# Optimization experiments

Hardware: AMD Instinct MI355X
Metric: run time of the kernel (lower is better)

The kernel has to match this reference:

```python
import jax, jax.numpy as jnp
import numpy as np

HEADS = 8
DIM_HEAD = 64
SCALE = DIM_HEAD ** -0.5


def setup_inputs() -> dict:
    key = jax.random.key(0)
    k1, k2, k3 = jax.random.split(key, 3)
    b, n, dim = 2, 4096, 512
    inner = HEADS * DIM_HEAD
    x = jax.random.normal(k1, (b, n, dim), dtype=jnp.float32)
    w_qkv = jax.random.normal(k2, (dim, 3 * inner), dtype=jnp.float32) * (dim ** -0.5)
    w_out = jax.random.normal(k3, (inner, dim), dtype=jnp.float32) * (inner ** -0.5)
    b_out = jnp.zeros((dim,), dtype=jnp.float32)
    return {"x": x, "w_qkv": w_qkv, "w_out": w_out, "b_out": b_out}


def reference(x, w_qkv, w_out, b_out):
    b, n, dim = x.shape
    qkv = x @ w_qkv  # [b, n, 3*inner]
    q, k, v = jnp.split(qkv, 3, axis=-1)
    # b n (h d) -> b h n d
    split_heads = lambda t: t.reshape(b, n, HEADS, DIM_HEAD).transpose(0, 2, 1, 3)
    q, k, v = split_heads(q), split_heads(k), split_heads(v)
    dots = jnp.einsum('bhid,bhjd->bhij', q, k) * SCALE  # [b, h, n, n]
    attn = jax.nn.log_softmax(dots, axis=-1)  # NOTE: log-softmax, not softmax
    out = jnp.einsum('bhij,bhjd->bhid', attn, v)  # [b, h, n, d]
    out = out.transpose(0, 2, 1, 3).reshape(b, n, HEADS * DIM_HEAD)
    return out @ w_out + b_out + x
```

## Files before the change

kernel.cpp:

```cpp
#include <hip/hip_runtime.h>
#include <stdint.h>

#define NSEQ   4096
#define BATCH  2
#define NHEAD  8
#define DHEAD  64
#define DIM    512
#define NQKV   1536
#define MROWS  (BATCH*NSEQ)
#define NBH    (BATCH*NHEAD)

typedef float  f32x4 __attribute__((ext_vector_type(4)));
typedef short  s16x8 __attribute__((ext_vector_type(8)));

__device__ __forceinline__ unsigned short f2b(float f){
  unsigned int u = __float_as_uint(f);
  u += 0x7FFFu + ((u >> 16) & 1u);
  return (unsigned short)(u >> 16);
}
__device__ __forceinline__ float b2f(unsigned short h){
  return __uint_as_float(((unsigned int)h) << 16);
}
__device__ __forceinline__ void gld_lds16(const void* g, void* l){
  __builtin_amdgcn_global_load_lds((const __attribute__((address_space(1))) unsigned int*)g,
                                   (__attribute__((address_space(3))) unsigned int*)l, 16, 0, 0);
}

__global__ void k_prep(const float* __restrict__ x, unsigned short* __restrict__ xb,
                       const float* __restrict__ wqkv, unsigned short* __restrict__ wqT,
                       const float* __restrict__ wout, unsigned short* __restrict__ woT){
  __shared__ float t[32][33];
  const int b = blockIdx.x;
  if (b < 4096){
    const int i = b*256 + threadIdx.x;
    float4 v = ((const float4*)x)[i];
    ushort4 o;
    o.x = f2b(v.x); o.y = f2b(v.y); o.z = f2b(v.z); o.w = f2b(v.w);
    ((ushort4*)xb)[i] = o;
  } else {
    const float* in; unsigned short* out; int R, C, cb, rb;
    if (b < 4096 + 768){
      const int q = b - 4096; in = wqkv; out = wqT; R = DIM; C = NQKV;
      cb = (q % 48)*32; rb = (q / 48)*32;
    } else {
      const int q = b - 4096 - 768; in = wout; out = woT; R = DIM; C = DIM;
      cb = (q & 15)*32; rb = (q >> 4)*32;
    }
    const int tx = threadIdx.x & 31, ty = threadIdx.x >> 5;
    #pragma unroll
    for (int s = 0; s < 32; s += 8) t[ty+s][tx] = in[(size_t)(rb+ty+s)*C + cb + tx];
    __syncthreads();
    #pragma unroll
    for (int s = 0; s < 32; s += 8) out[(size_t)(cb+ty+s)*R + rb + tx] = f2b(t[tx][ty+s]);
  }
}

#define QSTAGE(KS, B) do{ \
    const int k0_ = (KS)*32; \
    _Pragma("unroll") \
    for (int i_ = 0; i_ < 2; ++i_){ \
      const int slot_ = w*2 + i_; \
      const int r_ = slot_*16 + (lane>>2); \
      const int ch_ = (lane&3) ^ (r_&3); \
      gld_lds16(A  + (size_t)(m0+r_)*DIM + k0_ + ch_*8, (char*)at[B] + slot_*1024); \
      gld_lds16(Bt + (size_t)(n0+r_)*DIM + k0_ + ch_*8, (char*)bt[B] + slot_*1024); \
    }}while(0)

__global__ __launch_bounds__(256) void k_qkv_gemm(
    const unsigned short* __restrict__ A,
    const unsigned short* __restrict__ Bt,
    unsigned short* __restrict__ qbuf, unsigned short* __restrict__ kbuf,
    unsigned short* __restrict__ vbuf){
  __shared__ __align__(16) unsigned short at[2][128*32];
  __shared__ __align__(16) unsigned short bt[2][128*32];
  const int n0 = blockIdx.x*128, m0 = blockIdx.y*128;
  const int tid = threadIdx.x, w = tid>>6, lane = tid&63;
  const int wr = (w>>1)*64, wc = (w&1)*64;
  f32x4 acc[4][4] = {};
  QSTAGE(0, 0);
  for (int ks = 0; ks < 16; ++ks){
    __syncthreads();
    if (ks < 15) QSTAGE(ks+1, (ks+1)&1);
    const unsigned short* atc = at[ks&1];
    const unsigned short* btc = bt[ks&1];
    s16x8 af[4], bfr[4];
    #pragma unroll
    for (int f = 0; f < 4; ++f){
      const int rr = wr + f*16 + (lane&15);
      af[f]  = *(const s16x8*)((const char*)atc + rr*64 + ((((lane>>4)) ^ (rr&3))<<4));
      const int cc = wc + f*16 + (lane&15);
      bfr[f] = *(const s16x8*)((const char*)btc + cc*64 + ((((lane>>4)) ^ (cc&3))<<4));
    }
    #pragma unroll
    for (int fr = 0; fr < 4; ++fr)
      #pragma unroll
      for (int fc = 0; fc < 4; ++fc)
        acc[fr][fc] = __builtin_amdgcn_mfma_f32_16x16x32_bf16(bfr[fc], af[fr], acc[fr][fc], 0,0,0);
  }
  const float QS = 0.18033688011112042f;
  #pragma unroll
  for (int fr = 0; fr < 4; ++fr){
    const int row = m0 + wr + fr*16 + (lane&15);
    const int b = row >> 12, n = row & 4095;
    #pragma unroll
    for (int fc = 0; fc < 4; ++fc){
      const int col0 = n0 + wc + fc*16 + ((lane>>4)<<2);
      const int which = col0 >> 9;
      const int h = (col0 & 511) >> 6;
      const int d = col0 & 63;
      unsigned short* dst = (which==0) ? qbuf : ((which==1) ? kbuf : vbuf);
      const float sc = (which==0) ? QS : 1.f;
      ushort4 o;
      o.x = f2b(acc[fr][fc][0]*sc);
      o.y = f2b(acc[fr][fc][1]*sc);
      o.z = f2b(acc[fr][fc][2]*sc);
      o.w = f2b(acc[fr][fc][3]*sc);
      *(ushort4*)(dst + (size_t)((b*NHEAD + h)*NSEQ + n)*DHEAD + d) = o;
    }
  }
}

__global__ __launch_bounds__(256) void k_tpart(
    const unsigned short* __restrict__ kbuf, const unsigned short* __restrict__ vbuf,
    unsigned short* __restrict__ tpart, float* __restrict__ vsp){
  __shared__ __align__(16) unsigned short kt[64*64];
  __shared__ __align__(16) unsigned short vt[64*64];
  const int bh = blockIdx.y, jc = blockIdx.x;
  const unsigned short* K = kbuf + (size_t)bh*NSEQ*DHEAD;
  const unsigned short* V = vbuf + (size_t)bh*NSEQ*DHEAD;
  const int tid = threadIdx.x;
  const int d1 = (tid>>4)<<2, d2 = (tid&15)<<2;
  const int j0 = jc*64;
  #pragma unroll
  for (int c = 0; c < 2; ++c){
    const int q = tid + 256*c;
    const int row = q>>3, ch = q&7;
    *(float4*)((char*)kt + row*128 + ch*16) = *(const float4*)((const char*)K + (size_t)(j0+row)*128 + ch*16);
    *(float4*)((char*)vt + row*128 + ch*16) = *(const float4*)((const char*)V + (size_t)(j0+row)*128 + ch*16);
  }
  __syncthreads();
  float accT[4][4] = {{0.f}};
  float accV[4] = {0.f,0.f,0.f,0.f};
  for (int jj = 0; jj < 64; ++jj){
    const ushort4 k4 = *(const ushort4*)(kt + jj*64 + d1);
    const ushort4 v4 = *(const ushort4*)(vt + jj*64 + d2);
    float kf[4] = {b2f(k4.x), b2f(k4.y), b2f(k4.z), b2f(k4.w)};
    float vf[4] = {b2f(v4.x), b2f(v4.y), b2f(v4.z), b2f(v4.w)};
    #pragma unroll
    for (int a = 0; a < 4; ++a)
      #pragma unroll
      for (int b = 0; b < 4; ++b) accT[a][b] += kf[a]*vf[b];
    #pragma unroll
    for (int b = 0; b < 4; ++b) accV[b] += vf[b];
  }
  unsigned short* tp = tpart + ((size_t)bh*64 + jc)*4096;
  #pragma unroll
  for (int a = 0; a < 4; ++a)
    #pragma unroll
    for (int b = 0; b < 4; ++b) tp[(d1+a)*64 + (d2+b)] = f2b(accT[a][b]);
  if (tid < 16){
    #pragma unroll
    for (int b = 0; b < 4; ++b) vsp[((size_t)bh*64 + jc)*64 + d2 + b] = accV[b];
  }
}

__global__ void k_tred(const unsigned short* __restrict__ tpart, const float* __restrict__ vsp,
                       unsigned short* __restrict__ TB, float* __restrict__ vsum){
  const int blk = blockIdx.x;
  const int bh = blk >> 4, part = blk & 15;
  const int tid = threadIdx.x;
  const int idx = part*256 + tid;
  const int dd1 = idx>>6, dd2 = idx&63;
  float s = 0.f;
  #pragma unroll 8
  for (int pr = 0; pr < 64; ++pr) s += b2f(tpart[((size_t)bh*64 + pr)*4096 + idx]);
  TB[(size_t)bh*4096 + dd2*64 + dd1] = f2b(s);
  if (part == 0 && tid < 64){
    float v = 0.f;
    #pragma unroll 8
    for (int pr = 0; pr < 64; ++pr) v += vsp[((size_t)bh*64 + pr)*64 + tid];
    vsum[bh*64 + tid] = v;
  }
}

#define ASTAGE(U, BUFI) do { \
    const int ti_ = jbase + (((U)+phase)&15); \
    const size_t o_ = (size_t)ti_*64*DHEAD; \
    char* d_ = (char*)kt[BUFI]; \
    gld_lds16(kg0 + o_, d_ + s0*1024); \
    gld_lds16(kg1 + o_, d_ + s1*1024); } while(0)

#define ATILE(BUF) do { \
    const char* buf_ = (const char*)(BUF); \
    _Pragma("unroll") \
    for (int kk = 0; kk < 4; ++kk){ \
      const int r_ = kk*16 + (lane&15); \
      const s16x8 b0_ = *(const s16x8*)(buf_ + r_*128 + ((((lane>>4))   ^ (r_&7))<<4)); \
      const s16x8 b1_ = *(const s16x8*)(buf_ + r_*128 + (((4+(lane>>4)) ^ (r_&7))<<4)); \
      f32x4 a0_ = {0.f,0.f,0.f,0.f}, a1_ = {0.f,0.f,0.f,0.f}; \
      f32x4 a2_ = {0.f,0.f,0.f,0.f}, a3_ = {0.f,0.f,0.f,0.f}; \
      __builtin_amdgcn_s_setprio(1); \
      a0_ = __builtin_amdgcn_mfma_f32_16x16x32_bf16(aq[0][0], b0_, a0_, 0,0,0); \
      a0_ = __builtin_amdgcn_mfma_f32_16x16x32_bf16(aq[0][1], b1_, a0_, 0,0,0); \
      a1_ = __builtin_amdgcn_mfma_f32_16x16x32_bf16(aq[1][0], b0_, a1_, 0,0,0); \
      a1_ = __builtin_amdgcn_mfma_f32_16x16x32_bf16(aq[1][1], b1_, a1_, 0,0,0); \
      a2_ = __builtin_amdgcn_mfma_f32_16x16x32_bf16(aq[2][0], b0_, a2_, 0,0,0); \
      a2_ = __builtin_amdgcn_mfma_f32_16x16x32_bf16(aq[2][1], b1_, a2_, 0,0,0); \
      a3_ = __builtin_amdgcn_mfma_f32_16x16x32_bf16(aq[3][0], b0_, a3_, 0,0,0); \
      a3_ = __builtin_amdgcn_mfma_f32_16x16x32_bf16(aq[3][1], b1_, a3_, 0,0,0); \
      __builtin_amdgcn_s_setprio(0); \
      _Pragma("unroll") \
      for (int rr = 0; rr < 4; ++rr){ \
        lsum[0][rr] += __builtin_amdgcn_exp2f(a0_[rr]); \
        lsum[1][rr] += __builtin_amdgcn_exp2f(a1_[rr]); \
        lsum[2][rr] += __builtin_amdgcn_exp2f(a2_[rr]); \
        lsum[3][rr] += __builtin_amdgcn_exp2f(a3_[rr]); \
      } \
    } } while(0)

#define APHASE(U, LASTW) do { \
    if (LASTW) { asm volatile("s_waitcnt vmcnt(0)" ::: "memory"); } \
    else       { asm volatile("s_waitcnt vmcnt(2)" ::: "memory"); } \
    __builtin_amdgcn_s_barrier(); \
    asm volatile("" ::: "memory"); \
    if ((U) < 14) ASTAGE((U)+2, ((U)+2)&3); \
    ATILE(kt[(U)&3]); } while(0)

__global__ __launch_bounds__(256) void k_attn(
    const unsigned short* __restrict__ qbuf, const unsigned short* __restrict__ kbuf,
    float* __restrict__ ps){
  __shared__ __align__(16) unsigned short kt[4][64*64];
  const int bid = blockIdx.x;
  const int idx = bid >> 3;
  const int bh  = ((bid & 7) << 1) + (idx >> 6);
  const int rest = idx & 63;
  const int qchunk = rest >> 2;
  const int js = rest & 3;
  const int tid = threadIdx.x, w = tid>>6, lane = tid&63;
  const int q0 = qchunk*256 + w*64;
  const unsigned short* Q = qbuf + (size_t)bh*NSEQ*DHEAD;
  const unsigned short* K = kbuf + (size_t)bh*NSEQ*DHEAD;

  s16x8 aq[4][2];
  #pragma unroll
  for (int g = 0; g < 4; ++g){
    const int qrow = q0 + g*16 + (lane&15);
    aq[g][0] = *(const s16x8*)(Q + (size_t)qrow*DHEAD + ((lane>>4)<<3));
    aq[g][1] = *(const s16x8*)(Q + (size_t)qrow*DHEAD + 32 + ((lane>>4)<<3));
  }

  const int s0 = w*2, s1 = w*2 + 1;
  const int srow0 = s0*8 + (lane>>3), srow1 = s1*8 + (lane>>3);
  const int sch = ((lane&7) ^ (lane>>3));
  const unsigned short* kg0 = K + (size_t)srow0*DHEAD + sch*8;
  const unsigned short* kg1 = K + (size_t)srow1*DHEAD + sch*8;

  const int phase = (idx*5) & 15;
  const int jbase = js*16;

  ASTAGE(0, 0);
  ASTAGE(1, 1);

  float lsum[4][4] = {};
  APHASE(0,false);  APHASE(1,false);  APHASE(2,false);  APHASE(3,false);
  APHASE(4,false);  APHASE(5,false);  APHASE(6,false);  APHASE(7,false);
  APHASE(8,false);  APHASE(9,false);  APHASE(10,false); APHASE(11,false);
  APHASE(12,false); APHASE(13,false); APHASE(14,false); APHASE(15,true);

  #pragma unroll
  for (int m = 1; m < 16; m <<= 1)
    #pragma unroll
    for (int g = 0; g < 4; ++g)
      #pragma unroll
      for (int r = 0; r < 4; ++r) lsum[g][r] += __shfl_xor(lsum[g][r], m, 16);

  if ((lane&15) == 0){
    float* pp = ps + ((size_t)js*NBH + bh)*NSEQ;
    #pragma unroll
    for (int g = 0; g < 4; ++g)
      #pragma unroll
      for (int r = 0; r < 4; ++r)
        pp[q0 + g*16 + (lane>>4)*4 + r] = lsum[g][r];
  }
}

__global__ __launch_bounds__(256) void k_attn_fin(
    const unsigned short* __restrict__ qbuf, const unsigned short* __restrict__ TB,
    const float* __restrict__ vsum, const float* __restrict__ ps,
    unsigned short* __restrict__ om){
  const int bid = blockIdx.x;
  const int bh = bid >> 6, qchunk = bid & 63;
  const int tid = threadIdx.x, w = tid>>6, lane = tid&63;
  const int q0 = qchunk*64 + w*16;
  const unsigned short* Q = qbuf + (size_t)bh*NSEQ*DHEAD;
  const int qrow = q0 + (lane&15);
  const s16x8 aq0 = *(const s16x8*)(Q + (size_t)qrow*DHEAD + ((lane>>4)<<3));
  const s16x8 aq1 = *(const s16x8*)(Q + (size_t)qrow*DHEAD + 32 + ((lane>>4)<<3));
  const float* p0 = ps + (size_t)bh*NSEQ;
  const float* p1 = ps + ((size_t)NBH   + bh)*NSEQ;
  const float* p2 = ps + ((size_t)2*NBH + bh)*NSEQ;
  const float* p3 = ps + ((size_t)3*NBH + bh)*NSEQ;
  float lse2[4];
  #pragma unroll
  for (int r = 0; r < 4; ++r){
    const int n = q0 + (lane>>4)*4 + r;
    lse2[r] = log2f((p0[n] + p1[n]) + (p2[n] + p3[n]));
  }
  const unsigned short* tb = TB + (size_t)bh*4096;
  const int b = bh>>3, h = bh&7;
  #pragma unroll
  for (int fc = 0; fc < 4; ++fc){
    const int d2 = fc*16 + (lane&15);
    const s16x8 t0 = *(const s16x8*)(tb + d2*64 + ((lane>>4)<<3));
    const s16x8 t1 = *(const s16x8*)(tb + d2*64 + 32 + ((lane>>4)<<3));
    const float vs = vsum[bh*64 + d2];
    f32x4 acc = {0.f,0.f,0.f,0.f};
    acc = __builtin_amdgcn_mfma_f32_16x16x32_bf16(aq0, t0, acc, 0,0,0);
    acc = __builtin_amdgcn_mfma_f32_16x16x32_bf16(aq1, t1, acc, 0,0,0);
    #pragma unroll
    for (int r = 0; r < 4; ++r){
      const int n = q0 + (lane>>4)*4 + r;
      const float val = 0.6931471805599453f * (acc[r] - lse2[r]*vs);
      om[((size_t)b*NSEQ + n)*DIM + h*DHEAD + d2] = f2b(val);
    }
  }
}

#define OSTAGE(KS, B) do{ \
    const int k0_ = (KS)*32; \
    _Pragma("unroll") \
    for (int i_ = 0; i_ < 2; ++i_){ \
      const int slot_ = w*2 + i_; \
      const int r_ = slot_*16 + (lane>>2); \
      const int ch_ = (lane&3) ^ (r_&3); \
      gld_lds16(A  + (size_t)(m0+r_)*DIM + k0_ + ch_*8, (char*)at[B] + slot_*1024); \
      gld_lds16(Bt + (size_t)(n0+r_)*DIM + k0_ + ch_*8, (char*)bt[B] + slot_*1024); \
    }}while(0)

__global__ __launch_bounds__(256) void k_out_gemm(
    const unsigned short* __restrict__ A,
    const unsigned short* __restrict__ Bt,
    const float* __restrict__ bias, const float* __restrict__ xres,
    float* __restrict__ out){
  __shared__ __align__(16) unsigned short at[2][128*32];
  __shared__ __align__(16) unsigned short bt[2][128*32];
  const int n0 = blockIdx.x*128, m0 = blockIdx.y*128;
  const int tid = threadIdx.x, w = tid>>6, lane = tid&63;
  const int wr = (w>>1)*64, wc = (w&1)*64;
  f32x4 acc[4][4] = {};
  OSTAGE(0, 0);
  for (int ks = 0; ks < 16; ++ks){
    __syncthreads();
    if (ks < 15) OSTAGE(ks+1, (ks+1)&1);
    const unsigned short* atc = at[ks&1];
    const unsigned short* btc = bt[ks&1];
    s16x8 af[4], bfr[4];
    #pragma unroll
    for (int f = 0; f < 4; ++f){
      const int rr = wr + f*16 + (lane&15);
      af[f]  = *(const s16x8*)((const char*)atc + rr*64 + ((((lane>>4)) ^ (rr&3))<<4));
      const int cc = wc + f*16 + (lane&15);
      bfr[f] = *(const s16x8*)((const char*)btc + cc*64 + ((((lane>>4)) ^ (cc&3))<<4));
    }
    #pragma unroll
    for (int fr = 0; fr < 4; ++fr)
      #pragma unroll
      for (int fc = 0; fc < 4; ++fc)
        acc[fr][fc] = __builtin_amdgcn_mfma_f32_16x16x32_bf16(bfr[fc], af[fr], acc[fr][fc], 0,0,0);
  }
  #pragma unroll
  for (int fr = 0; fr < 4; ++fr){
    const int row = m0 + wr + fr*16 + (lane&15);
    #pragma unroll
    for (int fc = 0; fc < 4; ++fc){
      const int col0 = n0 + wc + fc*16 + ((lane>>4)<<2);
      const float4 bb = *(const float4*)&bias[col0];
      const float4 xr = *(const float4*)&xres[(size_t)row*DIM + col0];
      float4 o;
      o.x = acc[fr][fc][0] + bb.x + xr.x;
      o.y = acc[fr][fc][1] + bb.y + xr.y;
      o.z = acc[fr][fc][2] + bb.z + xr.z;
      o.w = acc[fr][fc][3] + bb.w + xr.w;
      *(float4*)&out[(size_t)row*DIM + col0] = o;
    }
  }
}

extern "C" void kernel_launch(void* const* d_in, const int* in_sizes, int n_in,
                              void* d_out, int out_size, void* d_ws, size_t ws_size,
                              hipStream_t stream){
  const float* x    = (const float*)d_in[0];
  const float* wqkv = (const float*)d_in[1];
  const float* wout = (const float*)d_in[2];
  const float* bout = (const float*)d_in[3];
  float* out = (float*)d_out;

  char* p = (char*)d_ws;
  unsigned short* xb   = (unsigned short*)p; p += (size_t)MROWS*DIM*2;
  unsigned short* wqT  = (unsigned short*)p; p += (size_t)NQKV*DIM*2;
  unsigned short* woT  = (unsigned short*)p; p += (size_t)DIM*DIM*2;
  unsigned short* qbuf = (unsigned short*)p; p += (size_t)NBH*NSEQ*DHEAD*2;
  unsigned short* kbuf = (unsigned short*)p; p += (size_t)NBH*NSEQ*DHEAD*2;
  unsigned short* vbuf = (unsigned short*)p; p += (size_t)NBH*NSEQ*DHEAD*2;
  unsigned short* tpart= (unsigned short*)p; p += (size_t)NBH*64*4096*2;
  float* vsp           = (float*)p;          p += (size_t)NBH*64*64*4;
  unsigned short* TB   = (unsigned short*)p; p += (size_t)NBH*64*64*2;
  float* vsum          = (float*)p;          p += (size_t)NBH*64*4;
  unsigned short* om   = (unsigned short*)p; p += (size_t)MROWS*DIM*2;
  float* ps            = (float*)p;          p += (size_t)4*NBH*NSEQ*4;

  k_prep<<<dim3(4096 + 768 + 256), dim3(256), 0, stream>>>(x, xb, wqkv, wqT, wout, woT);
  k_qkv_gemm<<<dim3(NQKV/128, MROWS/128), dim3(256), 0, stream>>>(xb, wqT, qbuf, kbuf, vbuf);
  k_tpart<<<dim3(64, NBH), dim3(256), 0, stream>>>(kbuf, vbuf, tpart, vsp);
  k_tred<<<dim3(256), dim3(256), 0, stream>>>(tpart, vsp, TB, vsum);
  k_attn<<<dim3(1024), dim3(256), 0, stream>>>(qbuf, kbuf, ps);
  k_attn_fin<<<dim3(1024), dim3(256), 0, stream>>>(qbuf, TB, vsum, ps, om);
  k_out_gemm<<<dim3(DIM/128, MROWS/128), dim3(256), 0, stream>>>(om, woT, bout, x, out);
}
```

Before: 127.6 us.

## Fold K^T V into output projection and merge attention with tpart launch

Merges the K^T·V partial-product kernel into the attention log-sum-exp kernel as a second block type in one launch, so both run concurrently. Removes the attn_fin kernel and its intermediate output matrix by precomputing G = (K^T V)·W_out per batch and head plus a vsum·W_out correction vector. The output GEMM then multiplies Q directly by G and subtracts the per-head LSE-weighted correction in its epilogue. This saves a launch and a full activation round-trip, but adds a small gmat kernel, extra bf16 rounding of G, and a heterogeneous block mix in one grid.

```diff
diff --git a/kernel.cpp b/kernel.cpp
--- a/kernel.cpp
+++ b/kernel.cpp
@@ -120,78 +120,15 @@
   }
 }
 
-__global__ __launch_bounds__(256) void k_tpart(
-    const unsigned short* __restrict__ kbuf, const unsigned short* __restrict__ vbuf,
-    unsigned short* __restrict__ tpart, float* __restrict__ vsp){
-  __shared__ __align__(16) unsigned short kt[64*64];
-  __shared__ __align__(16) unsigned short vt[64*64];
-  const int bh = blockIdx.y, jc = blockIdx.x;
-  const unsigned short* K = kbuf + (size_t)bh*NSEQ*DHEAD;
-  const unsigned short* V = vbuf + (size_t)bh*NSEQ*DHEAD;
-  const int tid = threadIdx.x;
-  const int d1 = (tid>>4)<<2, d2 = (tid&15)<<2;
-  const int j0 = jc*64;
-  #pragma unroll
-  for (int c = 0; c < 2; ++c){
-    const int q = tid + 256*c;
-    const int row = q>>3, ch = q&7;
-    *(float4*)((char*)kt + row*128 + ch*16) = *(const float4*)((const char*)K + (size_t)(j0+row)*128 + ch*16);
-    *(float4*)((char*)vt + row*128 + ch*16) = *(const float4*)((const char*)V + (size_t)(j0+row)*128 + ch*16);
-  }
-  __syncthreads();
-  float accT[4][4] = {{0.f}};
-  float accV[4] = {0.f,0.f,0.f,0.f};
-  for (int jj = 0; jj < 64; ++jj){
-    const ushort4 k4 = *(const ushort4*)(kt + jj*64 + d1);
-    const ushort4 v4 = *(const ushort4*)(vt + jj*64 + d2);
-    float kf[4] = {b2f(k4.x), b2f(k4.y), b2f(k4.z), b2f(k4.w)};
-    float vf[4] = {b2f(v4.x), b2f(v4.y), b2f(v4.z), b2f(v4.w)};
-    #pragma unroll
-    for (int a = 0; a < 4; ++a)
-      #pragma unroll
-      for (int b = 0; b < 4; ++b) accT[a][b] += kf[a]*vf[b];
-    #pragma unroll
-    for (int b = 0; b < 4; ++b) accV[b] += vf[b];
-  }
-  unsigned short* tp = tpart + ((size_t)bh*64 + jc)*4096;
-  #pragma unroll
-  for (int a = 0; a < 4; ++a)
-    #pragma unroll
-    for (int b = 0; b < 4; ++b) tp[(d1+a)*64 + (d2+b)] = f2b(accT[a][b]);
-  if (tid < 16){
-    #pragma unroll
-    for (int b = 0; b < 4; ++b) vsp[((size_t)bh*64 + jc)*64 + d2 + b] = accV[b];
-  }
-}
-
-__global__ void k_tred(const unsigned short* __restrict__ tpart, const float* __restrict__ vsp,
-                       unsigned short* __restrict__ TB, float* __restrict__ vsum){
-  const int blk = blockIdx.x;
-  const int bh = blk >> 4, part = blk & 15;
-  const int tid = threadIdx.x;
-  const int idx = part*256 + tid;
-  const int dd1 = idx>>6, dd2 = idx&63;
-  float s = 0.f;
-  #pragma unroll 8
-  for (int pr = 0; pr < 64; ++pr) s += b2f(tpart[((size_t)bh*64 + pr)*4096 + idx]);
-  TB[(size_t)bh*4096 + dd2*64 + dd1] = f2b(s);
-  if (part == 0 && tid < 64){
-    float v = 0.f;
-    #pragma unroll 8
-    for (int pr = 0; pr < 64; ++pr) v += vsp[((size_t)bh*64 + pr)*64 + tid];
-    vsum[bh*64 + tid] = v;
-  }
-}
-
 #define ASTAGE(U, BUFI) do { \
     const int ti_ = jbase + (((U)+phase)&15); \
     const size_t o_ = (size_t)ti_*64*DHEAD; \
-    char* d_ = (char*)kt[BUFI]; \
+    char* d_ = (char*)kt + (BUFI)*8192; \
     gld_lds16(kg0 + o_, d_ + s0*1024); \
     gld_lds16(kg1 + o_, d_ + s1*1024); } while(0)
 
-#define ATILE(BUF) do { \
-    const char* buf_ = (const char*)(BUF); \
+#define ATILE(BUFI) do { \
+    const char* buf_ = (const char*)kt + (BUFI)*8192; \
     _Pragma("unroll") \
     for (int kk = 0; kk < 4; ++kk){ \
       const int r_ = kk*16 + (lane&15); \
@@ -224,134 +161,235 @@
     __builtin_amdgcn_s_barrier(); \
     asm volatile("" ::: "memory"); \
     if ((U) < 14) ASTAGE((U)+2, ((U)+2)&3); \
-    ATILE(kt[(U)&3]); } while(0)
-
-__global__ __launch_bounds__(256) void k_attn(
+    ATILE((U)&3); } while(0)
+
+__global__ __launch_bounds__(256) void k_attn2(
     const unsigned short* __restrict__ qbuf, const unsigned short* __restrict__ kbuf,
-    float* __restrict__ ps){
-  __shared__ __align__(16) unsigned short kt[4][64*64];
+    const unsigned short* __restrict__ vbuf, float* __restrict__ ps,
+    unsigned short* __restrict__ tpart, float* __restrict__ vsp){
+  __shared__ __align__(16) char smem[32768];
+  const int bid0 = blockIdx.x;
+  const int grp = bid0 >> 4, which = (bid0 >> 3) & 1, l8 = bid0 & 7;
+  const int tid = threadIdx.x;
+
+  if (which == 0){
+    const int bid = grp*8 + l8;
+    unsigned short* kt = (unsigned short*)smem;
+    const int idx = bid >> 3;
+    const int bh  = ((bid & 7) << 1) + (idx >> 6);
+    const int rest = idx & 63;
+    const int qchunk = rest >> 2;
+    const int js = rest & 3;
+    const int w = tid>>6, lane = tid&63;
+    const int q0 = qchunk*256 + w*64;
+    const unsigned short* Q = qbuf + (size_t)bh*NSEQ*DHEAD;
+    const unsigned short* K = kbuf + (size_t)bh*NSEQ*DHEAD;
+
+    s16x8 aq[4][2];
+    #pragma unroll
+    for (int g = 0; g < 4; ++g){
+      const int qrow = q0 + g*16 + (lane&15);
+      aq[g][0] = *(const s16x8*)(Q + (size_t)qrow*DHEAD + ((lane>>4)<<3));
+      aq[g][1] = *(const s16x8*)(Q + (size_t)qrow*DHEAD + 32 + ((lane>>4)<<3));
+    }
+
+    const int s0 = w*2, s1 = w*2 + 1;
+    const int srow0 = s0*8 + (lane>>3), srow1 = s1*8 + (lane>>3);
+    const int sch = ((lane&7) ^ (lane>>3));
+    const unsigned short* kg0 = K + (size_t)srow0*DHEAD + sch*8;
+    const unsigned short* kg1 = K + (size_t)srow1*DHEAD + sch*8;
+
+    const int phase = (idx*5) & 15;
+    const int jbase = js*16;
+
+    ASTAGE(0, 0);
+    ASTAGE(1, 1);
+
+    float lsum[4][4] = {};
+    APHASE(0,false);  APHASE(1,false);  APHASE(2,false);  APHASE(3,false);
+    APHASE(4,false);  APHASE(5,false);  APHASE(6,false);  APHASE(7,false);
+    APHASE(8,false);  APHASE(9,false);  APHASE(10,false); APHASE(11,false);
+    APHASE(12,false); APHASE(13,false); APHASE(14,false); APHASE(15,true);
+
+    #pragma unroll
+    for (int m = 1; m < 16; m <<= 1)
+      #pragma unroll
+      for (int g = 0; g < 4; ++g)
+        #pragma unroll
+        for (int r = 0; r < 4; ++r) lsum[g][r] += __shfl_xor(lsum[g][r], m, 16);
+
+    if ((lane&15) == 0){
+      float* pp = ps + ((size_t)js*NBH + bh)*NSEQ;
+      #pragma unroll
+      for (int g = 0; g < 4; ++g)
+        #pragma unroll
+        for (int r = 0; r < 4; ++r)
+          pp[q0 + g*16 + (lane>>4)*4 + r] = lsum[g][r];
+    }
+  } else {
+    const int t = grp*8 + l8;
+    const int bh = t >> 6, jc = t & 63;
+    unsigned short* kt = (unsigned short*)smem;
+    unsigned short* vt = (unsigned short*)(smem + 8192);
+    const unsigned short* K = kbuf + (size_t)bh*NSEQ*DHEAD;
+    const unsigned short* V = vbuf + (size_t)bh*NSEQ*DHEAD;
+    const int d1 = (tid>>4)<<2, d2 = (tid&15)<<2;
+    const int j0 = jc*64;
+    #pragma unroll
+    for (int c = 0; c < 2; ++c){
+      const int q = tid + 256*c;
+      const int row = q>>3, ch = q&7;
+      *(float4*)((char*)kt + row*128 + ch*16) = *(const float4*)((const char*)K + (size_t)(j0+row)*128 + ch*16);
+      *(float4*)((char*)vt + row*128 + ch*16) = *(const float4*)((const char*)V + (size_t)(j0+row)*128 + ch*16);
+    }
+    __syncthreads();
+    float accT[4][4] = {{0.f}};
+    float accV[4] = {0.f,0.f,0.f,0.f};
+    for (int jj = 0; jj < 64; ++jj){
+      const ushort4 k4 = *(const ushort4*)(kt + jj*64 + d1);
+      const ushort4 v4 = *(const ushort4*)(vt + jj*64 + d2);
+      float kf[4] = {b2f(k4.x), b2f(k4.y), b2f(k4.z), b2f(k4.w)};
+      float vf[4] = {b2f(v4.x), b2f(v4.y), b2f(v4.z), b2f(v4.w)};
+      #pragma unroll
+      for (int a = 0; a < 4; ++a)
+        #pragma unroll
+        for (int b = 0; b < 4; ++b) accT[a][b] += kf[a]*vf[b];
+      #pragma unroll
+      for (int b = 0; b < 4; ++b) accV[b] += vf[b];
+    }
+    unsigned short* tp = tpart + ((size_t)bh*64 + jc)*4096;
+    #pragma unroll
+    for (int a = 0; a < 4; ++a)
+      #pragma unroll
+      for (int b = 0; b < 4; ++b) tp[(d1+a)*64 + (d2+b)] = f2b(accT[a][b]);
+    if (tid < 16){
+      #pragma unroll
+      for (int b = 0; b < 4; ++b) vsp[((size_t)bh*64 + jc)*64 + d2 + b] = accV[b];
+    }
+  }
+}
+
+__global__ void k_tred(const unsigned short* __restrict__ tpart, const float* __restrict__ vsp,
+                       unsigned short* __restrict__ TB, float* __restrict__ vsum){
+  const int blk = blockIdx.x;
+  const int bh = blk >> 4, part = blk & 15;
+  const int tid = threadIdx.x;
+  const int idx = part*256 + tid;
+  const int dd1 = idx>>6, dd2 = idx&63;
+  float s = 0.f;
+  #pragma unroll 8
+  for (int pr = 0; pr < 64; ++pr) s += b2f(tpart[((size_t)bh*64 + pr)*4096 + idx]);
+  TB[(size_t)bh*4096 + dd2*64 + dd1] = f2b(s);
+  if (part == 0 && tid < 64){
+    float v = 0.f;
+    #pragma unroll 8
+    for (int pr = 0; pr < 64; ++pr) v += vsp[((size_t)bh*64 + pr)*64 + tid];
+    vsum[bh*64 + tid] = v;
+  }
+}
+
+__global__ __launch_bounds__(256) void k_gmat(
+    const unsigned short* __restrict__ TB, const float* __restrict__ vsum,
+    const unsigned short* __restrict__ woT,
+    unsigned short* __restrict__ Gt, float* __restrict__ vw){
+  __shared__ __align__(16) unsigned short Tsh[64*64];
+  __shared__ __align__(16) unsigned short wsh[64*64];
   const int bid = blockIdx.x;
-  const int idx = bid >> 3;
-  const int bh  = ((bid & 7) << 1) + (idx >> 6);
-  const int rest = idx & 63;
-  const int qchunk = rest >> 2;
-  const int js = rest & 3;
-  const int tid = threadIdx.x, w = tid>>6, lane = tid&63;
-  const int q0 = qchunk*256 + w*64;
-  const unsigned short* Q = qbuf + (size_t)bh*NSEQ*DHEAD;
-  const unsigned short* K = kbuf + (size_t)bh*NSEQ*DHEAD;
-
-  s16x8 aq[4][2];
+  const int b = bid >> 6, h = (bid >> 3) & 7, ct = bid & 7;
+  const int bh = b*8 + h, c0 = ct*64;
+  const int tid = threadIdx.x;
+  {
+    const unsigned short* src = TB + (size_t)bh*4096;
+    *(s16x8*)&Tsh[tid*16]     = *(const s16x8*)&src[tid*16];
+    *(s16x8*)&Tsh[tid*16 + 8] = *(const s16x8*)&src[tid*16 + 8];
+  }
+  {
+    const int c = tid & 63, d2b = (tid >> 6) << 4;
+    const unsigned short* wr = woT + (size_t)(c0+c)*DIM + h*64 + d2b;
+    s16x8 w0 = *(const s16x8*)wr;
+    s16x8 w1 = *(const s16x8*)(wr+8);
+    #pragma unroll
+    for (int i = 0; i < 8; ++i){
+      wsh[(d2b+i)*64 + c]   = w0[i];
+      wsh[(d2b+8+i)*64 + c] = w1[i];
+    }
+  }
+  __syncthreads();
+  const int d1 = (tid>>4)<<2, cc = (tid&15)<<2;
+  float accG[4][4] = {{0.f}};
+  for (int d2 = 0; d2 < 64; ++d2){
+    const ushort4 tv = *(const ushort4*)&Tsh[d2*64 + d1];
+    const ushort4 wv = *(const ushort4*)&wsh[d2*64 + cc];
+    float tf[4] = {b2f(tv.x), b2f(tv.y), b2f(tv.z), b2f(tv.w)};
+    float wf[4] = {b2f(wv.x), b2f(wv.y), b2f(wv.z), b2f(wv.w)};
+    #pragma unroll
+    for (int a = 0; a < 4; ++a)
+      #pragma unroll
+      for (int bb = 0; bb < 4; ++bb) accG[a][bb] += tf[a]*wf[bb];
+  }
+  const float LN2 = 0.6931471805599453f;
+  unsigned short* G = Gt + ((size_t)b*DIM + c0)*DIM + h*64;
   #pragma unroll
-  for (int g = 0; g < 4; ++g){
-    const int qrow = q0 + g*16 + (lane&15);
-    aq[g][0] = *(const s16x8*)(Q + (size_t)qrow*DHEAD + ((lane>>4)<<3));
-    aq[g][1] = *(const s16x8*)(Q + (size_t)qrow*DHEAD + 32 + ((lane>>4)<<3));
-  }
-
-  const int s0 = w*2, s1 = w*2 + 1;
-  const int srow0 = s0*8 + (lane>>3), srow1 = s1*8 + (lane>>3);
-  const int sch = ((lane&7) ^ (lane>>3));
-  const unsigned short* kg0 = K + (size_t)srow0*DHEAD + sch*8;
-  const unsigned short* kg1 = K + (size_t)srow1*DHEAD + sch*8;
-
-  const int phase = (idx*5) & 15;
-  const int jbase = js*16;
-
-  ASTAGE(0, 0);
-  ASTAGE(1, 1);
-
-  float lsum[4][4] = {};
-  APHASE(0,false);  APHASE(1,false);  APHASE(2,false);  APHASE(3,false);
-  APHASE(4,false);  APHASE(5,false);  APHASE(6,false);  APHASE(7,false);
-  APHASE(8,false);  APHASE(9,false);  APHASE(10,false); APHASE(11,false);
-  APHASE(12,false); APHASE(13,false); APHASE(14,false); APHASE(15,true);
-
-  #pragma unroll
-  for (int m = 1; m < 16; m <<= 1)
-    #pragma unroll
-    for (int g = 0; g < 4; ++g)
-      #pragma unroll
-      for (int r = 0; r < 4; ++r) lsum[g][r] += __shfl_xor(lsum[g][r], m, 16);
-
-  if ((lane&15) == 0){
-    float* pp = ps + ((size_t)js*NBH + bh)*NSEQ;
-    #pragma unroll
-    for (int g = 0; g < 4; ++g)
-      #pragma unroll
-      for (int r = 0; r < 4; ++r)
-        pp[q0 + g*16 + (lane>>4)*4 + r] = lsum[g][r];
-  }
-}
-
-__global__ __launch_bounds__(256) void k_attn_fin(
-    const unsigned short* __restrict__ qbuf, const unsigned short* __restrict__ TB,
-    const float* __restrict__ vsum, const float* __restrict__ ps,
-    unsigned short* __restrict__ om){
-  const int bid = blockIdx.x;
-  const int bh = bid >> 6, qchunk = bid & 63;
-  const int tid = threadIdx.x, w = tid>>6, lane = tid&63;
-  const int q0 = qchunk*64 + w*16;
-  const unsigned short* Q = qbuf + (size_t)bh*NSEQ*DHEAD;
-  const int qrow = q0 + (lane&15);
-  const s16x8 aq0 = *(const s16x8*)(Q + (size_t)qrow*DHEAD + ((lane>>4)<<3));
-  const s16x8 aq1 = *(const s16x8*)(Q + (size_t)qrow*DHEAD + 32 + ((lane>>4)<<3));
-  const float* p0 = ps + (size_t)bh*NSEQ;
-  const float* p1 = ps + ((size_t)NBH   + bh)*NSEQ;
-  const float* p2 = ps + ((size_t)2*NBH + bh)*NSEQ;
-  const float* p3 = ps + ((size_t)3*NBH + bh)*NSEQ;
-  float lse2[4];
-  #pragma unroll
-  for (int r = 0; r < 4; ++r){
-    const int n = q0 + (lane>>4)*4 + r;
-    lse2[r] = log2f((p0[n] + p1[n]) + (p2[n] + p3[n]));
-  }
-  const unsigned short* tb = TB + (size_t)bh*4096;
-  const int b = bh>>3, h = bh&7;
-  #pragma unroll
-  for (int fc = 0; fc < 4; ++fc){
-    const int d2 = fc*16 + (lane&15);
-    const s16x8 t0 = *(const s16x8*)(tb + d2*64 + ((lane>>4)<<3));
-    const s16x8 t1 = *(const s16x8*)(tb + d2*64 + 32 + ((lane>>4)<<3));
-    const float vs = vsum[bh*64 + d2];
-    f32x4 acc = {0.f,0.f,0.f,0.f};
-    acc = __builtin_amdgcn_mfma_f32_16x16x32_bf16(aq0, t0, acc, 0,0,0);
-    acc = __builtin_amdgcn_mfma_f32_16x16x32_bf16(aq1, t1, acc, 0,0,0);
-    #pragma unroll
-    for (int r = 0; r < 4; ++r){
-      const int n = q0 + (lane>>4)*4 + r;
-      const float val = 0.6931471805599453f * (acc[r] - lse2[r]*vs);
-      om[((size_t)b*NSEQ + n)*DIM + h*DHEAD + d2] = f2b(val);
-    }
-  }
-}
-
-#define OSTAGE(KS, B) do{ \
-    const int k0_ = (KS)*32; \
+  for (int bb = 0; bb < 4; ++bb)
+    #pragma unroll
+    for (int a = 0; a < 4; ++a)
+      G[(size_t)(cc+bb)*DIM + d1 + a] = f2b(accG[a][bb]*LN2);
+  if (tid < 64){
+    float s = 0.f;
+    for (int d2 = 0; d2 < 64; ++d2) s += vsum[bh*64 + d2]*b2f(wsh[d2*64 + tid]);
+    vw[(size_t)bh*DIM + c0 + tid] = s*LN2;
+  }
+}
+
+#define FSTAGE(KS, B) do{ \
+    const int k0_ = (KS)*32; const int h_ = k0_>>6; const int kk_ = k0_&63; \
     _Pragma("unroll") \
     for (int i_ = 0; i_ < 2; ++i_){ \
       const int slot_ = w*2 + i_; \
       const int r_ = slot_*16 + (lane>>2); \
       const int ch_ = (lane&3) ^ (r_&3); \
-      gld_lds16(A  + (size_t)(m0+r_)*DIM + k0_ + ch_*8, (char*)at[B] + slot_*1024); \
-      gld_lds16(Bt + (size_t)(n0+r_)*DIM + k0_ + ch_*8, (char*)bt[B] + slot_*1024); \
+      gld_lds16(Aq + ((size_t)h_*NSEQ + mrow0 + r_)*DHEAD + kk_ + ch_*8, (char*)at[B] + slot_*1024); \
+      gld_lds16(Gb + (size_t)(n0+r_)*DIM + k0_ + ch_*8, (char*)bt[B] + slot_*1024); \
     }}while(0)
 
 __global__ __launch_bounds__(256) void k_out_gemm(
-    const unsigned short* __restrict__ A,
-    const unsigned short* __restrict__ Bt,
+    const unsigned short* __restrict__ qbuf,
+    const unsigned short* __restrict__ Gt,
+    const float* __restrict__ vw,
+    const float* __restrict__ ps,
     const float* __restrict__ bias, const float* __restrict__ xres,
     float* __restrict__ out){
   __shared__ __align__(16) unsigned short at[2][128*32];
   __shared__ __align__(16) unsigned short bt[2][128*32];
+  __shared__ float Lsh[128][9];
+  __shared__ float vwsh[8][128];
   const int n0 = blockIdx.x*128, m0 = blockIdx.y*128;
+  const int b = m0 >> 12, mrow0 = m0 & 4095;
   const int tid = threadIdx.x, w = tid>>6, lane = tid&63;
   const int wr = (w>>1)*64, wc = (w&1)*64;
+  const unsigned short* Aq = qbuf + (size_t)b*NHEAD*NSEQ*DHEAD;
+  const unsigned short* Gb = Gt + (size_t)b*DIM*DIM;
+
   f32x4 acc[4][4] = {};
-  OSTAGE(0, 0);
+  FSTAGE(0, 0);
+
+  {
+    const int rl = tid >> 1, h0 = (tid & 1) << 2;
+    #pragma unroll
+    for (int i = 0; i < 4; ++i){
+      const int h = h0 + i;
+      const float* pp = ps + (size_t)(b*NHEAD + h)*NSEQ + mrow0 + rl;
+      const float s = (pp[0] + pp[(size_t)NBH*NSEQ]) +
+                      (pp[(size_t)2*NBH*NSEQ] + pp[(size_t)3*NBH*NSEQ]);
+      Lsh[rl][h] = log2f(s);
+    }
+    const int hh = tid >> 5, cl = (tid & 31) << 2;
+    *(float4*)&vwsh[hh][cl] = *(const float4*)&vw[(size_t)(b*NHEAD + hh)*DIM + n0 + cl];
+  }
+
   for (int ks = 0; ks < 16; ++ks){
     __syncthreads();
-    if (ks < 15) OSTAGE(ks+1, (ks+1)&1);
+    if (ks < 15) FSTAGE(ks+1, (ks+1)&1);
     const unsigned short* atc = at[ks&1];
     const unsigned short* btc = bt[ks&1];
     s16x8 af[4], bfr[4];
@@ -368,19 +406,35 @@
       for (int fc = 0; fc < 4; ++fc)
         acc[fr][fc] = __builtin_amdgcn_mfma_f32_16x16x32_bf16(bfr[fc], af[fr], acc[fr][fc], 0,0,0);
   }
+
+  float Lv[4][8];
+  #pragma unroll
+  for (int fr = 0; fr < 4; ++fr){
+    const int rl = wr + fr*16 + (lane&15);
+    #pragma unroll
+    for (int h = 0; h < 8; ++h) Lv[fr][h] = Lsh[rl][h];
+  }
   #pragma unroll
   for (int fr = 0; fr < 4; ++fr){
     const int row = m0 + wr + fr*16 + (lane&15);
     #pragma unroll
     for (int fc = 0; fc < 4; ++fc){
-      const int col0 = n0 + wc + fc*16 + ((lane>>4)<<2);
+      const int cl0 = wc + fc*16 + ((lane>>4)<<2);
+      const int col0 = n0 + cl0;
+      float4 corr = {0.f,0.f,0.f,0.f};
+      #pragma unroll
+      for (int h = 0; h < 8; ++h){
+        const float4 vv = *(const float4*)&vwsh[h][cl0];
+        const float lh = Lv[fr][h];
+        corr.x += lh*vv.x; corr.y += lh*vv.y; corr.z += lh*vv.z; corr.w += lh*vv.w;
+      }
       const float4 bb = *(const float4*)&bias[col0];
       const float4 xr = *(const float4*)&xres[(size_t)row*DIM + col0];
       float4 o;
-      o.x = acc[fr][fc][0] + bb.x + xr.x;
-      o.y = acc[fr][fc][1] + bb.y + xr.y;
-      o.z = acc[fr][fc][2] + bb.z + xr.z;
-      o.w = acc[fr][fc][3] + bb.w + xr.w;
+      o.x = acc[fr][fc][0] - corr.x + bb.x + xr.x;
+      o.y = acc[fr][fc][1] - corr.y + bb.y + xr.y;
+      o.z = acc[fr][fc][2] - corr.z + bb.z + xr.z;
+      o.w = acc[fr][fc][3] - corr.w + bb.w + xr.w;
       *(float4*)&out[(size_t)row*DIM + col0] = o;
     }
   }
@@ -406,14 +460,14 @@
   float* vsp           = (float*)p;          p += (size_t)NBH*64*64*4;
   unsigned short* TB   = (unsigned short*)p; p += (size_t)NBH*64*64*2;
   float* vsum          = (float*)p;          p += (size_t)NBH*64*4;
-  unsigned short* om   = (unsigned short*)p; p += (size_t)MROWS*DIM*2;
+  unsigned short* Gt   = (unsigned short*)p; p += (size_t)2*DIM*DIM*2;
+  float* vw            = (float*)p;          p += (size_t)NBH*DIM*4;
   float* ps            = (float*)p;          p += (size_t)4*NBH*NSEQ*4;
 
   k_prep<<<dim3(4096 + 768 + 256), dim3(256), 0, stream>>>(x, xb, wqkv, wqT, wout, woT);
   k_qkv_gemm<<<dim3(NQKV/128, MROWS/128), dim3(256), 0, stream>>>(xb, wqT, qbuf, kbuf, vbuf);
-  k_tpart<<<dim3(64, NBH), dim3(256), 0, stream>>>(kbuf, vbuf, tpart, vsp);
+  k_attn2<<<dim3(2048), dim3(256), 0, stream>>>(qbuf, kbuf, vbuf, ps, tpart, vsp);
   k_tred<<<dim3(256), dim3(256), 0, stream>>>(tpart, vsp, TB, vsum);
-  k_attn<<<dim3(1024), dim3(256), 0, stream>>>(qbuf, kbuf, ps);
-  k_attn_fin<<<dim3(1024), dim3(256), 0, stream>>>(qbuf, TB, vsum, ps, om);
-  k_out_gemm<<<dim3(DIM/128, MROWS/128), dim3(256), 0, stream>>>(om, woT, bout, x, out);
-}
+  k_gmat<<<dim3(128), dim3(256), 0, stream>>>(TB, vsum, woT, Gt, vw);
+  k_out_gemm<<<dim3(DIM/128, MROWS/128), dim3(256), 0, stream>>>(qbuf, Gt, vw, ps, bout, x, out);
+}
```

Result: slower. 155.9 us (+22.2%).

## Deepen attention K prefetch to three stages and coarsen K^T V partials

Applied to the files above, without the earlier changes.

The attention row-sum kernel now keeps three K tiles in flight instead of two, with vmcnt waits adjusted, to better hide global-to-LDS load latency across its four LDS buffers. Separately, the K^T·V partial kernel now processes four 64-row chunks per block (16 blocks per head instead of 64), writing fp32 partials with vectorized stores. This shrinks the partial buffer and the reduction loop in k_tred and removes a bf16 rounding step, at the cost of fewer blocks and more serial work per block in k_tpart.

```diff
diff --git a/kernel.cpp b/kernel.cpp
--- a/kernel.cpp
+++ b/kernel.cpp
@@ -122,7 +122,7 @@
 
 __global__ __launch_bounds__(256) void k_tpart(
     const unsigned short* __restrict__ kbuf, const unsigned short* __restrict__ vbuf,
-    unsigned short* __restrict__ tpart, float* __restrict__ vsp){
+    float* __restrict__ tpartf, float* __restrict__ vsp){
   __shared__ __align__(16) unsigned short kt[64*64];
   __shared__ __align__(16) unsigned short vt[64*64];
   const int bh = blockIdx.y, jc = blockIdx.x;
@@ -130,41 +130,45 @@
   const unsigned short* V = vbuf + (size_t)bh*NSEQ*DHEAD;
   const int tid = threadIdx.x;
   const int d1 = (tid>>4)<<2, d2 = (tid&15)<<2;
-  const int j0 = jc*64;
-  #pragma unroll
-  for (int c = 0; c < 2; ++c){
-    const int q = tid + 256*c;
-    const int row = q>>3, ch = q&7;
-    *(float4*)((char*)kt + row*128 + ch*16) = *(const float4*)((const char*)K + (size_t)(j0+row)*128 + ch*16);
-    *(float4*)((char*)vt + row*128 + ch*16) = *(const float4*)((const char*)V + (size_t)(j0+row)*128 + ch*16);
-  }
-  __syncthreads();
   float accT[4][4] = {{0.f}};
   float accV[4] = {0.f,0.f,0.f,0.f};
-  for (int jj = 0; jj < 64; ++jj){
-    const ushort4 k4 = *(const ushort4*)(kt + jj*64 + d1);
-    const ushort4 v4 = *(const ushort4*)(vt + jj*64 + d2);
-    float kf[4] = {b2f(k4.x), b2f(k4.y), b2f(k4.z), b2f(k4.w)};
-    float vf[4] = {b2f(v4.x), b2f(v4.y), b2f(v4.z), b2f(v4.w)};
-    #pragma unroll
-    for (int a = 0; a < 4; ++a)
-      #pragma unroll
-      for (int b = 0; b < 4; ++b) accT[a][b] += kf[a]*vf[b];
-    #pragma unroll
-    for (int b = 0; b < 4; ++b) accV[b] += vf[b];
-  }
-  unsigned short* tp = tpart + ((size_t)bh*64 + jc)*4096;
-  #pragma unroll
-  for (int a = 0; a < 4; ++a)
-    #pragma unroll
-    for (int b = 0; b < 4; ++b) tp[(d1+a)*64 + (d2+b)] = f2b(accT[a][b]);
+  for (int st = 0; st < 4; ++st){
+    const int j0 = jc*256 + st*64;
+    __syncthreads();
+    #pragma unroll
+    for (int c = 0; c < 2; ++c){
+      const int q = tid + 256*c;
+      const int row = q>>3, ch = q&7;
+      *(float4*)((char*)kt + row*128 + ch*16) = *(const float4*)((const char*)K + (size_t)(j0+row)*128 + ch*16);
+      *(float4*)((char*)vt + row*128 + ch*16) = *(const float4*)((const char*)V + (size_t)(j0+row)*128 + ch*16);
+    }
+    __syncthreads();
+    for (int jj = 0; jj < 64; ++jj){
+      const ushort4 k4 = *(const ushort4*)(kt + jj*64 + d1);
+      const ushort4 v4 = *(const ushort4*)(vt + jj*64 + d2);
+      float kf[4] = {b2f(k4.x), b2f(k4.y), b2f(k4.z), b2f(k4.w)};
+      float vf[4] = {b2f(v4.x), b2f(v4.y), b2f(v4.z), b2f(v4.w)};
+      #pragma unroll
+      for (int a = 0; a < 4; ++a)
+        #pragma unroll
+        for (int b = 0; b < 4; ++b) accT[a][b] += kf[a]*vf[b];
+      #pragma unroll
+      for (int b = 0; b < 4; ++b) accV[b] += vf[b];
+    }
+  }
+  float* tp = tpartf + ((size_t)bh*16 + jc)*4096;
+  #pragma unroll
+  for (int a = 0; a < 4; ++a){
+    float4 o; o.x = accT[a][0]; o.y = accT[a][1]; o.z = accT[a][2]; o.w = accT[a][3];
+    *(float4*)&tp[(d1+a)*64 + d2] = o;
+  }
   if (tid < 16){
     #pragma unroll
-    for (int b = 0; b < 4; ++b) vsp[((size_t)bh*64 + jc)*64 + d2 + b] = accV[b];
-  }
-}
-
-__global__ void k_tred(const unsigned short* __restrict__ tpart, const float* __restrict__ vsp,
+    for (int b = 0; b < 4; ++b) vsp[((size_t)bh*16 + jc)*64 + d2 + b] = accV[b];
+  }
+}
+
+__global__ void k_tred(const float* __restrict__ tpartf, const float* __restrict__ vsp,
                        unsigned short* __restrict__ TB, float* __restrict__ vsum){
   const int blk = blockIdx.x;
   const int bh = blk >> 4, part = blk & 15;
@@ -172,13 +176,13 @@
   const int idx = part*256 + tid;
   const int dd1 = idx>>6, dd2 = idx&63;
   float s = 0.f;
-  #pragma unroll 8
-  for (int pr = 0; pr < 64; ++pr) s += b2f(tpart[((size_t)bh*64 + pr)*4096 + idx]);
+  #pragma unroll
+  for (int pr = 0; pr < 16; ++pr) s += tpartf[((size_t)bh*16 + pr)*4096 + idx];
   TB[(size_t)bh*4096 + dd2*64 + dd1] = f2b(s);
   if (part == 0 && tid < 64){
     float v = 0.f;
-    #pragma unroll 8
-    for (int pr = 0; pr < 64; ++pr) v += vsp[((size_t)bh*64 + pr)*64 + tid];
+    #pragma unroll
+    for (int pr = 0; pr < 16; ++pr) v += vsp[((size_t)bh*16 + pr)*64 + tid];
     vsum[bh*64 + tid] = v;
   }
 }
@@ -190,8 +194,8 @@
     gld_lds16(kg0 + o_, d_ + s0*1024); \
     gld_lds16(kg1 + o_, d_ + s1*1024); } while(0)
 
-#define ATILE(BUF) do { \
-    const char* buf_ = (const char*)(BUF); \
+#define ATILE(BUFI) do { \
+    const char* buf_ = (const char*)kt[BUFI]; \
     _Pragma("unroll") \
     for (int kk = 0; kk < 4; ++kk){ \
       const int r_ = kk*16 + (lane&15); \
@@ -218,13 +222,14 @@
       } \
     } } while(0)
 
-#define APHASE(U, LASTW) do { \
-    if (LASTW) { asm volatile("s_waitcnt vmcnt(0)" ::: "memory"); } \
-    else       { asm volatile("s_waitcnt vmcnt(2)" ::: "memory"); } \
+#define APHASE(U) do { \
+    if ((U) <= 13)      { asm volatile("s_waitcnt vmcnt(4)" ::: "memory"); } \
+    else if ((U) == 14) { asm volatile("s_waitcnt vmcnt(2)" ::: "memory"); } \
+    else                { asm volatile("s_waitcnt vmcnt(0)" ::: "memory"); } \
     __builtin_amdgcn_s_barrier(); \
     asm volatile("" ::: "memory"); \
-    if ((U) < 14) ASTAGE((U)+2, ((U)+2)&3); \
-    ATILE(kt[(U)&3]); } while(0)
+    if ((U) <= 12) ASTAGE((U)+3, ((U)+3)&3); \
+    ATILE((U)&3); } while(0)
 
 __global__ __launch_bounds__(256) void k_attn(
     const unsigned short* __restrict__ qbuf, const unsigned short* __restrict__ kbuf,
@@ -260,12 +265,13 @@
 
   ASTAGE(0, 0);
   ASTAGE(1, 1);
+  ASTAGE(2, 2);
 
   float lsum[4][4] = {};
-  APHASE(0,false);  APHASE(1,false);  APHASE(2,false);  APHASE(3,false);
-  APHASE(4,false);  APHASE(5,false);  APHASE(6,false);  APHASE(7,false);
-  APHASE(8,false);  APHASE(9,false);  APHASE(10,false); APHASE(11,false);
-  APHASE(12,false); APHASE(13,false); APHASE(14,false); APHASE(15,true);
+  APHASE(0);  APHASE(1);  APHASE(2);  APHASE(3);
+  APHASE(4);  APHASE(5);  APHASE(6);  APHASE(7);
+  APHASE(8);  APHASE(9);  APHASE(10); APHASE(11);
+  APHASE(12); APHASE(13); APHASE(14); APHASE(15);
 
   #pragma unroll
   for (int m = 1; m < 16; m <<= 1)
@@ -402,8 +408,8 @@
   unsigned short* qbuf = (unsigned short*)p; p += (size_t)NBH*NSEQ*DHEAD*2;
   unsigned short* kbuf = (unsigned short*)p; p += (size_t)NBH*NSEQ*DHEAD*2;
   unsigned short* vbuf = (unsigned short*)p; p += (size_t)NBH*NSEQ*DHEAD*2;
-  unsigned short* tpart= (unsigned short*)p; p += (size_t)NBH*64*4096*2;
-  float* vsp           = (float*)p;          p += (size_t)NBH*64*64*4;
+  float* tpartf        = (float*)p;          p += (size_t)NBH*16*4096*4;
+  float* vsp           = (float*)p;          p += (size_t)NBH*16*64*4;
   unsigned short* TB   = (unsigned short*)p; p += (size_t)NBH*64*64*2;
   float* vsum          = (float*)p;          p += (size_t)NBH*64*4;
   unsigned short* om   = (unsigned short*)p; p += (size_t)MROWS*DIM*2;
@@ -411,8 +417,8 @@
 
   k_prep<<<dim3(4096 + 768 + 256), dim3(256), 0, stream>>>(x, xb, wqkv, wqT, wout, woT);
   k_qkv_gemm<<<dim3(NQKV/128, MROWS/128), dim3(256), 0, stream>>>(xb, wqT, qbuf, kbuf, vbuf);
-  k_tpart<<<dim3(64, NBH), dim3(256), 0, stream>>>(kbuf, vbuf, tpart, vsp);
-  k_tred<<<dim3(256), dim3(256), 0, stream>>>(tpart, vsp, TB, vsum);
+  k_tpart<<<dim3(16, NBH), dim3(256), 0, stream>>>(kbuf, vbuf, tpartf, vsp);
+  k_tred<<<dim3(256), dim3(256), 0, stream>>>(tpartf, vsp, TB, vsum);
   k_attn<<<dim3(1024), dim3(256), 0, stream>>>(qbuf, kbuf, ps);
   k_attn_fin<<<dim3(1024), dim3(256), 0, stream>>>(qbuf, TB, vsum, ps, om);
   k_out_gemm<<<dim3(DIM/128, MROWS/128), dim3(256), 0, stream>>>(om, woT, bout, x, out);
```

Result: faster. 124.2 us (-2.6%).
